# Kernel tuning notes

Hardware: AMD Instinct MI355X
Metric: run time of the kernel (lower is better)

## Reference

```python
import jax, jax.numpy as jnp
import numpy as np


def setup_inputs() -> dict:
    key = jax.random.key(0)
    k1, k2, k3 = jax.random.split(key, 3)
    B, T, D, Uh = 64, 256, 1024, 1024
    x = jax.random.normal(k1, (B, T, D), dtype=jnp.float32)
    W = jax.random.normal(k2, (D, 4 * Uh), dtype=jnp.float32) * 0.02
    U = jax.random.normal(k3, (Uh, 4 * Uh), dtype=jnp.float32) * 0.02
    b = jnp.zeros((4 * Uh,), dtype=jnp.float32)
    return {"x": x, "W": W, "U": U, "b": b}


def _lstm(x, W, U, b):
    # Keras LSTM, inference mode (dropout inactive). Gate order: i, f, c, o.
    B = x.shape[0]
    units = U.shape[0]
    # Precompute input projection for all timesteps: [B,T,4U] -> scan over T.
    xz = jnp.einsum('btd,dg->btg', x, W) + b
    xz = jnp.swapaxes(xz, 0, 1)  # [T,B,4U]

    def step(carry, xz_t):
        h, c = carry
        z = xz_t + h @ U  # [B,4U]
        zi, zf, zg, zo = jnp.split(z, 4, axis=-1)
        i = jax.nn.sigmoid(zi)
        f = jax.nn.sigmoid(zf)
        g = jnp.tanh(zg)
        o = jax.nn.sigmoid(zo)
        c_new = f * c + i * g
        h_new = o * jnp.tanh(c_new)
        return (h_new, c_new), h_new

    h0 = jnp.zeros((B, units), dtype=x.dtype)
    c0 = jnp.zeros((B, units), dtype=x.dtype)
    _, hs = jax.lax.scan(step, (h0, c0), xz)  # hs: [T,B,U]
    return jnp.swapaxes(hs, 0, 1)  # [B,T,U] (return_sequences=True)


def reference(x, W, U, b):
    return _lstm(x, W, U, b)
```

## Files before the change

kernel.cpp:

```cpp
#include <hip/hip_runtime.h>
#include <cstdint>
#include <cstddef>

typedef __attribute__((ext_vector_type(8))) short short8;
typedef __attribute__((ext_vector_type(4))) short short4v;
typedef __attribute__((ext_vector_type(4))) float f32x4;
typedef __attribute__((ext_vector_type(4))) int int4v;

static constexpr int B_ = 64, T_ = 256, D_ = 1024, NH = 1024, NG = 4096;
static constexpr int NBLK = 64;
static constexpr int NWRK = 192;
static constexpr int LDS_BYTES = 131072 + 64 * 68 * 4;
static constexpr uint64_t DLY_TICKS = 50;

__device__ __forceinline__ short f2bs(float f) {
  union { float f; uint32_t u; } cv; cv.f = f;
  uint32_t u = cv.u;
  uint32_t r = (u + 0x7fffu + ((u >> 16) & 1u)) >> 16;
  return (short)(uint16_t)r;
}
__device__ __forceinline__ float bs2f(short s) {
  union { uint32_t u; float f; } cv; cv.u = ((uint32_t)(uint16_t)s) << 16; return cv.f;
}
__device__ __forceinline__ float fsigm(float x) {
  return __builtin_amdgcn_rcpf(1.f + __expf(-x));
}
__device__ __forceinline__ float ftanh(float x) {
  return 1.f - 2.f * __builtin_amdgcn_rcpf(__expf(2.f * x) + 1.f);
}
__device__ __forceinline__ uint64_t rtclock() {
  uint64_t v;
  asm volatile("s_memrealtime %0\n\ts_waitcnt lgkmcnt(0)" : "=s"(v));
  return v;
}

#define WAITV(N) do { asm volatile("s_waitcnt vmcnt(" #N ")" ::: "memory"); \
                      __builtin_amdgcn_sched_barrier(0); } while (0)

#define HL2(B0, B1, VO) \
  asm volatile("global_load_dwordx4 %0, %2, %3 sc0 sc1\n\t" \
               "global_load_dwordx4 %1, %2, %3 offset:16 sc0 sc1" \
               : "=&v"(B0), "=&v"(B1) : "v"(VO), "s"(hpv) : "memory")

#define ISSUE_A { _Pragma("unroll") \
  for (int K = 0; K < 8; ++K) HL2(bufA[2*K], bufA[2*K+1], voff0 + K * 8192); }
#define ISSUE_B { _Pragma("unroll") \
  for (int K = 0; K < 8; ++K) HL2(bufB[2*K], bufB[2*K+1], voff0 + 65536 + K * 8192); }

#define CHECKBUF(BUF) { _Pragma("unroll") \
  for (int i = 0; i < 16; ++i) { \
    bad |= ((uint32_t)BUF[i][0] ^ tgw); bad |= ((uint32_t)BUF[i][1] ^ tgw); \
    bad |= ((uint32_t)BUF[i][2] ^ tgw); bad |= ((uint32_t)BUF[i][3] ^ tgw); \
  } bad &= 0xFFFF0000u; }

#define MFMA_SUB(BUF, KB) { _Pragma("unroll") \
  for (int K = 0; K < 8; ++K) { \
    int4v pk; \
    pk[0] = (BUF[2*K][0]   & 0xFFFF) | (BUF[2*K][1]   << 16); \
    pk[1] = (BUF[2*K][2]   & 0xFFFF) | (BUF[2*K][3]   << 16); \
    pk[2] = (BUF[2*K+1][0] & 0xFFFF) | (BUF[2*K+1][1] << 16); \
    pk[3] = (BUF[2*K+1][2] & 0xFFFF) | (BUF[2*K+1][3] << 16); \
    const short8 fa = __builtin_bit_cast(short8, pk); \
    const int ksAbs = kh * 16 + (KB) + K; \
    _Pragma("unroll") \
    for (int nt = 0; nt < 4; ++nt) { \
      const short8 fb = *reinterpret_cast<const short8*>(&Us[((ksAbs*4 + kg)*64 + nt*16 + fr)*8]); \
      acc[nt] = __builtin_amdgcn_mfma_f32_16x16x32_bf16(fa, fb, acc[nt], 0, 0, 0); \
    } \
  } }

__global__ __launch_bounds__(512, 1) void lstm_fused(
    const float* __restrict__ x, const float* __restrict__ W,
    const float* __restrict__ bias, const float* __restrict__ U,
    short* __restrict__ xzT, uint32_t* __restrict__ h0buf,
    uint32_t* __restrict__ h1buf, int* __restrict__ ready,
    float* __restrict__ out)
{
  extern __shared__ char smem[];
  const int tid  = threadIdx.x;
  const int lane = tid & 63, wave = tid >> 6;
  const int bid  = blockIdx.x;
  const int fr = lane & 15, kg = lane >> 4;

  if (bid >= NBLK) {
    short* As = (short*)smem;
    short* Bs = (short*)(smem + 16384);
    short* Cs = (short*)smem;
    const int wm = (wave >> 2) * 128, wn = (wave & 3) * 64;
    const int fq = lane >> 4;
    const int wid = bid - NBLK;

    for (int tile = wid; tile < 1024; tile += NWRK) {
      const int tt = tile >> 4;
      const int bn = (tile & 15) * 256;
      f32x4 acc[8][4] = {};

      for (int k0 = 0; k0 < D_; k0 += 32) {
        {
          const int r0 = tid >> 3, kq = (tid & 7) * 4;
          #pragma unroll
          for (int it = 0; it < 4; ++it) {
            const int r = r0 + it * 64;
            const int m = tt * 256 + r;
            const int xr = (m & 63) * 256 + (m >> 6);
            const float4 v = *reinterpret_cast<const float4*>(&x[(size_t)xr * D_ + k0 + kq]);
            short4v s; s.x = f2bs(v.x); s.y = f2bs(v.y); s.z = f2bs(v.z); s.w = f2bs(v.w);
            *reinterpret_cast<short4v*>(&As[r * 32 + kq]) = s;
          }
        }
        {
          const int kr0 = tid >> 6, nq = (tid & 63) * 4;
          #pragma unroll
          for (int it = 0; it < 4; ++it) {
            const int krow = kr0 + it * 8;
            const float4 v = *reinterpret_cast<const float4*>(&W[(size_t)(k0 + krow) * NG + bn + nq]);
            short4v s; s.x = f2bs(v.x); s.y = f2bs(v.y); s.z = f2bs(v.z); s.w = f2bs(v.w);
            *reinterpret_cast<short4v*>(&Bs[krow * 256 + nq]) = s;
          }
        }
        __syncthreads();

        short8 af[8];
        #pragma unroll
        for (int mi = 0; mi < 8; ++mi)
          af[mi] = *reinterpret_cast<const short8*>(&As[(wm + mi * 16 + fr) * 32 + kg * 8]);
        #pragma unroll
        for (int ni = 0; ni < 4; ++ni) {
          short8 bf;
          #pragma unroll
          for (int j = 0; j < 8; ++j) bf[j] = Bs[(kg * 8 + j) * 256 + wn + ni * 16 + fr];
          #pragma unroll
          for (int mi = 0; mi < 8; ++mi)
            acc[mi][ni] = __builtin_amdgcn_mfma_f32_16x16x32_bf16(af[mi], bf, acc[mi][ni], 0, 0, 0);
        }
        __syncthreads();
      }

      const int g = bn >> 10, rb0 = (bn & 1023) >> 4;
      #pragma unroll
      for (int hp = 0; hp < 2; ++hp) {
        __syncthreads();
        if ((wave >> 2) == hp) {
          #pragma unroll
          for (int ni = 0; ni < 4; ++ni) {
            const int col = wn + ni * 16 + fr;
            const float bv = bias[bn + col];
            #pragma unroll
            for (int mi = 0; mi < 8; ++mi) {
              const int rowl = mi * 16 + fq * 4;
              #pragma unroll
              for (int r = 0; r < 4; ++r)
                Cs[(rowl + r) * 264 + col] = f2bs(acc[mi][ni][r] + bv);
            }
          }
        }
        __syncthreads();
        #pragma unroll
        for (int it = 0; it < 4; ++it) {
          const int cid = it * 512 + tid;
          const int tl = cid >> 4, rbi = cid & 15;
          const int r = hp * 128 + tl;
          const int t = tt * 4 + (r >> 6);
          const int b = r & 63;
          short* dst = xzT + ((size_t)((rb0 + rbi) * 256 + t) * 64 + b) * 64 + g * 16;
          const int4v v0 = *reinterpret_cast<const int4v*>(&Cs[tl * 264 + rbi * 16]);
          const int4v v1 = *reinterpret_cast<const int4v*>(&Cs[tl * 264 + rbi * 16 + 8]);
          asm volatile("global_store_dwordx4 %0, %1, off sc0 sc1\n\t"
                       "global_store_dwordx4 %0, %2, off offset:16 sc0 sc1"
                       :: "v"(dst), "v"(v0), "v"(v1) : "memory");
        }
      }
      asm volatile("s_waitcnt vmcnt(0)" ::: "memory");
      __syncthreads();
      if (tid == 0)
        __hip_atomic_fetch_add(&ready[tt], 1, __ATOMIC_RELAXED, __HIP_MEMORY_SCOPE_AGENT);
    }
    return;
  }

  short* Us  = (short*)smem;
  float* zsm = (float*)(smem + 131072);

  const int u0 = bid * 16;
  const int mt = wave & 3;
  const int kh = wave >> 2;
  const int gb = tid >> 3, gup = tid & 7;

  for (int idx = tid; idx < 1024 * 64; idx += 512) {
    const int k = idx >> 6, c = idx & 63;
    Us[((k >> 3) * 64 + c) * 8 + (k & 7)] =
        f2bs(U[(size_t)k * NG + (c >> 4) * NH + u0 + (c & 15)]);
  }
  float creg0 = 0.f, creg1 = 0.f;
  const int voff0 = kh * 131072 + kg * 2048 + mt * 512 + fr * 32;
  const int pks = bid >> 1;
  const int pkg = ((bid & 1) << 1) + (gup >> 2);
  const int pj  = (2 * gup) & 7;
  const int pidx = ((pks * 4 + pkg) * 64 + gb) * 8 + pj;
  __syncthreads();
  uint64_t rt0 = rtclock();
  int grpOK = -1;

  for (int t = 0; t < T_; ++t) {
    const uint32_t* __restrict__ hpv = (t & 1) ? h0buf : h1buf;
    uint32_t* __restrict__ hnx       = (t & 1) ? h1buf : h0buf;

    const int grp = t >> 4;
    if (grp > grpOK) {
      if (lane == 0) {
        int spun = 0;
        for (;;) {
          int4v rv;
          asm volatile("global_load_dwordx4 %0, %1, off sc0 sc1\n\t"
                       "s_waitcnt vmcnt(0)"
                       : "=&v"(rv) : "v"(ready + grp * 4) : "memory");
          if (rv[0] == 16 && rv[1] == 16 && rv[2] == 16 && rv[3] == 16) break;
          spun = 1;
          __builtin_amdgcn_s_sleep(16);
        }
        if (spun) {
          #pragma unroll
          for (int s = 0; s < 4; ++s) __builtin_amdgcn_s_sleep(127);
        }
      }
      grpOK = grp;
    }

    int xzw[4];
    {
      const short* xb = xzT + ((((size_t)bid * 256 + t) * 64 + gb) * 64 + 2 * gup);
      asm volatile("global_load_dword %0, %4, off sc0 sc1\n\t"
                   "global_load_dword %1, %4, off offset:32 sc0 sc1\n\t"
                   "global_load_dword %2, %4, off offset:64 sc0 sc1\n\t"
                   "global_load_dword %3, %4, off offset:96 sc0 sc1"
                   : "=&v"(xzw[0]), "=&v"(xzw[1]), "=&v"(xzw[2]), "=&v"(xzw[3])
                   : "v"(xb) : "memory");
    }

    f32x4 acc[4] = {};
    if (t > 0) {
      const uint32_t tgw = (uint32_t)t << 16;
      int4v bufA[16], bufB[16];
      while ((uint64_t)(rtclock() - rt0) < DLY_TICKS)
        __builtin_amdgcn_s_sleep(1);
      ISSUE_A; ISSUE_B;
      WAITV(16);
      for (;;) {
        uint32_t bad = 0; CHECKBUF(bufA);
        if (__all(bad == 0)) break;
        __builtin_amdgcn_s_sleep(4);
        ISSUE_A; WAITV(0);
      }
      MFMA_SUB(bufA, 0);
      WAITV(0);
      for (;;) {
        uint32_t bad = 0; CHECKBUF(bufB);
        if (__all(bad == 0)) break;
        __builtin_amdgcn_s_sleep(4);
        ISSUE_B; WAITV(0);
      }
      MFMA_SUB(bufB, 8);

      if (kh == 1) {
        #pragma unroll
        for (int nt = 0; nt < 4; ++nt)
          #pragma unroll
          for (int r = 0; r < 4; ++r)
            zsm[(mt * 16 + kg * 4 + r) * 68 + nt * 16 + fr] = acc[nt][r];
      }
      __syncthreads();
      if (kh == 0) {
        #pragma unroll
        for (int nt = 0; nt < 4; ++nt)
          #pragma unroll
          for (int r = 0; r < 4; ++r)
            zsm[(mt * 16 + kg * 4 + r) * 68 + nt * 16 + fr] += acc[nt][r];
      }
      __syncthreads();
    } else {
      asm volatile("s_waitcnt vmcnt(0)" ::: "memory");
    }

    {
      float z[4][2];
      #pragma unroll
      for (int g = 0; g < 4; ++g) {
        z[g][0] = bs2f((short)(xzw[g] & 0xFFFF));
        z[g][1] = bs2f((short)(((uint32_t)xzw[g]) >> 16));
        if (t > 0) {
          const float2 zz = *reinterpret_cast<const float2*>(&zsm[gb * 68 + g * 16 + 2 * gup]);
          z[g][0] += zz.x; z[g][1] += zz.y;
        }
      }
      float hh0, hh1;
      {
        const float ig = fsigm(z[0][0]), fg = fsigm(z[1][0]);
        const float gg = ftanh(z[2][0]), og = fsigm(z[3][0]);
        creg0 = fg * creg0 + ig * gg;  hh0 = og * ftanh(creg0);
      }
      {
        const float ig = fsigm(z[0][1]), fg = fsigm(z[1][1]);
        const float gg = ftanh(z[2][1]), og = fsigm(z[3][1]);
        creg1 = fg * creg1 + ig * gg;  hh1 = og * ftanh(creg1);
      }
      if (t < T_ - 1) {
        const uint32_t tgp = (uint32_t)(t + 1) << 16;
        const uint64_t hw64 =
            (uint64_t)(tgp | (uint32_t)(uint16_t)f2bs(hh0)) |
            ((uint64_t)(tgp | (uint32_t)(uint16_t)f2bs(hh1)) << 32);
        (void)__hip_atomic_exchange((uint64_t*)(hnx + pidx), hw64,
                                    __ATOMIC_RELAXED, __HIP_MEMORY_SCOPE_AGENT);
      }
      rt0 = rtclock();
      float2 o; o.x = hh0; o.y = hh1;
      *reinterpret_cast<float2*>(&out[((size_t)gb * T_ + t) * NH + u0 + 2 * gup]) = o;
    }
    __builtin_amdgcn_s_barrier();
  }
}

extern "C" void kernel_launch(void* const* d_in, const int* in_sizes, int n_in,
                              void* d_out, int out_size, void* d_ws, size_t ws_size,
                              hipStream_t stream) {
  const float* x    = (const float*)d_in[0];
  const float* W    = (const float*)d_in[1];
  const float* U    = (const float*)d_in[2];
  const float* bias = (const float*)d_in[3];
  float* out = (float*)d_out;
  char* ws = (char*)d_ws;

  short*    xzT   = (short*)ws;
  uint32_t* hA    = (uint32_t*)(ws + 134217728);
  uint32_t* hB    = (uint32_t*)(ws + 134217728 + 262144);
  int*      ready = (int*)(ws + 134217728 + 524288);

  hipMemsetAsync(ws + 134217728, 0, 524288 + 4096, stream);

  hipFuncSetAttribute((const void*)lstm_fused,
                      hipFuncAttributeMaxDynamicSharedMemorySize, LDS_BYTES);
  lstm_fused<<<dim3(NBLK + NWRK), dim3(512), LDS_BYTES, stream>>>(
      x, W, bias, U, xzT, hA, hB, ready, out);
}
```

Baseline: 1.918 ms.

## Quantize recurrent matmul to int8 and pin recurrent blocks to one XCD

The recurrent weights U and hidden state h move from bf16 to int8, using per-column scales for U and a fixed 127 scale for h, and the step matmul now uses i8 MFMA. This halves the h exchange payload and the LDS footprint. Recurrent roles are claimed dynamically only by blocks running on XCC 0, so all 64 recurrent blocks share one L2 and h reads use non-sc1 loads. The projection GEMM tiles shrink to 128 rows across more worker blocks that later become recurrent roles, and the launch allows 4 blocks per CU. The int8 quantization lowers accuracy, and the role-claim scheme relies on enough blocks landing on XCD 0.

```diff
diff --git a/kernel.cpp b/kernel.cpp
--- a/kernel.cpp
+++ b/kernel.cpp
@@ -6,12 +6,13 @@
 typedef __attribute__((ext_vector_type(4))) short short4v;
 typedef __attribute__((ext_vector_type(4))) float f32x4;
 typedef __attribute__((ext_vector_type(4))) int int4v;
+typedef __attribute__((ext_vector_type(2))) int int2v;
 
 static constexpr int B_ = 64, T_ = 256, D_ = 1024, NH = 1024, NG = 4096;
-static constexpr int NBLK = 64;
-static constexpr int NWRK = 192;
-static constexpr int LDS_BYTES = 131072 + 64 * 68 * 4;
-static constexpr uint64_t DLY_TICKS = 50;
+static constexpr int NROLE = 64;
+static constexpr int NWRK  = 448;
+static constexpr int LDS_BYTES = 65536 + 16384;
+static constexpr uint64_t DLY_TICKS = 25;
 
 __device__ __forceinline__ short f2bs(float f) {
   union { float f; uint32_t u; } cv; cv.f = f;
@@ -37,71 +38,90 @@
 #define WAITV(N) do { asm volatile("s_waitcnt vmcnt(" #N ")" ::: "memory"); \
                       __builtin_amdgcn_sched_barrier(0); } while (0)
 
-#define HL2(B0, B1, VO) \
-  asm volatile("global_load_dwordx4 %0, %2, %3 sc0 sc1\n\t" \
-               "global_load_dwordx4 %1, %2, %3 offset:16 sc0 sc1" \
-               : "=&v"(B0), "=&v"(B1) : "v"(VO), "s"(hpv) : "memory")
-
-#define ISSUE_A { _Pragma("unroll") \
-  for (int K = 0; K < 8; ++K) HL2(bufA[2*K], bufA[2*K+1], voff0 + K * 8192); }
-#define ISSUE_B { _Pragma("unroll") \
-  for (int K = 0; K < 8; ++K) HL2(bufB[2*K], bufB[2*K+1], voff0 + 65536 + K * 8192); }
+#define HLF(B0, VO) \
+  asm volatile("global_load_dwordx4 %0, %1, %2 sc0" \
+               : "=&v"(B0) : "v"(VO), "s"(hpv) : "memory")
+#define HLS(B0, VO) \
+  asm volatile("global_load_dwordx4 %0, %1, %2 sc0 sc1" \
+               : "=&v"(B0) : "v"(VO), "s"(hpv) : "memory")
+
+#define ISSUE_F(BUF, BASE) { _Pragma("unroll") \
+  for (int K = 0; K < 8; ++K) HLF(BUF[K], voff0 + (BASE) + K * 4096); }
+#define ISSUE_S(BUF, BASE) { _Pragma("unroll") \
+  for (int K = 0; K < 8; ++K) HLS(BUF[K], voff0 + (BASE) + K * 4096); }
 
 #define CHECKBUF(BUF) { _Pragma("unroll") \
-  for (int i = 0; i < 16; ++i) { \
+  for (int i = 0; i < 8; ++i) { \
     bad |= ((uint32_t)BUF[i][0] ^ tgw); bad |= ((uint32_t)BUF[i][1] ^ tgw); \
     bad |= ((uint32_t)BUF[i][2] ^ tgw); bad |= ((uint32_t)BUF[i][3] ^ tgw); \
   } bad &= 0xFFFF0000u; }
 
 #define MFMA_SUB(BUF, KB) { _Pragma("unroll") \
   for (int K = 0; K < 8; ++K) { \
-    int4v pk; \
-    pk[0] = (BUF[2*K][0]   & 0xFFFF) | (BUF[2*K][1]   << 16); \
-    pk[1] = (BUF[2*K][2]   & 0xFFFF) | (BUF[2*K][3]   << 16); \
-    pk[2] = (BUF[2*K+1][0] & 0xFFFF) | (BUF[2*K+1][1] << 16); \
-    pk[3] = (BUF[2*K+1][2] & 0xFFFF) | (BUF[2*K+1][3] << 16); \
-    const short8 fa = __builtin_bit_cast(short8, pk); \
+    int2v ad; \
+    ad[0] = (BUF[K][0] & 0xFFFF) | ((BUF[K][1] & 0xFFFF) << 16); \
+    ad[1] = (BUF[K][2] & 0xFFFF) | ((BUF[K][3] & 0xFFFF) << 16); \
+    const long long a64 = __builtin_bit_cast(long long, ad); \
     const int ksAbs = kh * 16 + (KB) + K; \
     _Pragma("unroll") \
     for (int nt = 0; nt < 4; ++nt) { \
-      const short8 fb = *reinterpret_cast<const short8*>(&Us[((ksAbs*4 + kg)*64 + nt*16 + fr)*8]); \
-      acc[nt] = __builtin_amdgcn_mfma_f32_16x16x32_bf16(fa, fb, acc[nt], 0, 0, 0); \
+      const int boff = ((ksAbs * 4 + kg) * 64 + nt * 16 + fr) * 8; \
+      const long long b64 = *reinterpret_cast<const long long*>(Us + boff); \
+      acc[nt] = __builtin_amdgcn_mfma_i32_16x16x32_i8(a64, b64, acc[nt], 0, 0, 0); \
     } \
   } }
 
-__global__ __launch_bounds__(512, 1) void lstm_fused(
+__global__ __launch_bounds__(512, 4) void lstm_mega(
     const float* __restrict__ x, const float* __restrict__ W,
     const float* __restrict__ bias, const float* __restrict__ U,
     short* __restrict__ xzT, uint32_t* __restrict__ h0buf,
     uint32_t* __restrict__ h1buf, int* __restrict__ ready,
-    float* __restrict__ out)
+    int* __restrict__ claim, float* __restrict__ out)
 {
   extern __shared__ char smem[];
   const int tid  = threadIdx.x;
   const int lane = tid & 63, wave = tid >> 6;
-  const int bid  = blockIdx.x;
   const int fr = lane & 15, kg = lane >> 4;
 
-  if (bid >= NBLK) {
+  int* role_sh = (int*)smem;
+  if (tid == 0) {
+    int xcd = 0;
+    asm volatile("s_getreg_b32 %0, hwreg(HW_REG_XCC_ID)" : "=s"(xcd));
+    int r = -1;
+    if ((xcd & 7) == 0)
+      r = __hip_atomic_fetch_add(claim, 1, __ATOMIC_RELAXED, __HIP_MEMORY_SCOPE_AGENT);
+    role_sh[0] = r;
+  }
+  __syncthreads();
+  int role = role_sh[0];
+  __syncthreads();
+
+  if (role < 0 || role >= NROLE) {
     short* As = (short*)smem;
-    short* Bs = (short*)(smem + 16384);
+    short* Bs = (short*)(smem + 8192);
     short* Cs = (short*)smem;
-    const int wm = (wave >> 2) * 128, wn = (wave & 3) * 64;
+    const int wm = (wave >> 2) * 64, wn = (wave & 3) * 64;
     const int fq = lane >> 4;
-    const int wid = bid - NBLK;
-
-    for (int tile = wid; tile < 1024; tile += NWRK) {
-      const int tt = tile >> 4;
+    int wid;
+    if (tid == 0)
+      role_sh[1] = __hip_atomic_fetch_add(claim + 4, 1, __ATOMIC_RELAXED,
+                                          __HIP_MEMORY_SCOPE_AGENT);
+    __syncthreads();
+    wid = role_sh[1];
+    __syncthreads();
+
+    for (int tile = wid; tile < 2048; tile += NWRK) {
+      const int mtile = tile >> 4;
       const int bn = (tile & 15) * 256;
-      f32x4 acc[8][4] = {};
+      f32x4 acc[4][4] = {};
 
       for (int k0 = 0; k0 < D_; k0 += 32) {
         {
           const int r0 = tid >> 3, kq = (tid & 7) * 4;
           #pragma unroll
-          for (int it = 0; it < 4; ++it) {
+          for (int it = 0; it < 2; ++it) {
             const int r = r0 + it * 64;
-            const int m = tt * 256 + r;
+            const int m = mtile * 128 + r;
             const int xr = (m & 63) * 256 + (m >> 6);
             const float4 v = *reinterpret_cast<const float4*>(&x[(size_t)xr * D_ + k0 + kq]);
             short4v s; s.x = f2bs(v.x); s.y = f2bs(v.y); s.z = f2bs(v.z); s.w = f2bs(v.w);
@@ -120,9 +140,9 @@
         }
         __syncthreads();
 
-        short8 af[8];
-        #pragma unroll
-        for (int mi = 0; mi < 8; ++mi)
+        short8 af[4];
+        #pragma unroll
+        for (int mi = 0; mi < 4; ++mi)
           af[mi] = *reinterpret_cast<const short8*>(&As[(wm + mi * 16 + fr) * 32 + kg * 8]);
         #pragma unroll
         for (int ni = 0; ni < 4; ++ni) {
@@ -130,74 +150,88 @@
           #pragma unroll
           for (int j = 0; j < 8; ++j) bf[j] = Bs[(kg * 8 + j) * 256 + wn + ni * 16 + fr];
           #pragma unroll
-          for (int mi = 0; mi < 8; ++mi)
+          for (int mi = 0; mi < 4; ++mi)
             acc[mi][ni] = __builtin_amdgcn_mfma_f32_16x16x32_bf16(af[mi], bf, acc[mi][ni], 0, 0, 0);
         }
         __syncthreads();
       }
 
       const int g = bn >> 10, rb0 = (bn & 1023) >> 4;
+      __syncthreads();
       #pragma unroll
-      for (int hp = 0; hp < 2; ++hp) {
-        __syncthreads();
-        if ((wave >> 2) == hp) {
-          #pragma unroll
-          for (int ni = 0; ni < 4; ++ni) {
-            const int col = wn + ni * 16 + fr;
-            const float bv = bias[bn + col];
-            #pragma unroll
-            for (int mi = 0; mi < 8; ++mi) {
-              const int rowl = mi * 16 + fq * 4;
-              #pragma unroll
-              for (int r = 0; r < 4; ++r)
-                Cs[(rowl + r) * 264 + col] = f2bs(acc[mi][ni][r] + bv);
-            }
-          }
-        }
-        __syncthreads();
-        #pragma unroll
-        for (int it = 0; it < 4; ++it) {
-          const int cid = it * 512 + tid;
-          const int tl = cid >> 4, rbi = cid & 15;
-          const int r = hp * 128 + tl;
-          const int t = tt * 4 + (r >> 6);
-          const int b = r & 63;
-          short* dst = xzT + ((size_t)((rb0 + rbi) * 256 + t) * 64 + b) * 64 + g * 16;
-          const int4v v0 = *reinterpret_cast<const int4v*>(&Cs[tl * 264 + rbi * 16]);
-          const int4v v1 = *reinterpret_cast<const int4v*>(&Cs[tl * 264 + rbi * 16 + 8]);
-          asm volatile("global_store_dwordx4 %0, %1, off sc0 sc1\n\t"
-                       "global_store_dwordx4 %0, %2, off offset:16 sc0 sc1"
-                       :: "v"(dst), "v"(v0), "v"(v1) : "memory");
-        }
+      for (int ni = 0; ni < 4; ++ni) {
+        const int col = wn + ni * 16 + fr;
+        const float bv = bias[bn + col];
+        #pragma unroll
+        for (int mi = 0; mi < 4; ++mi) {
+          const int rowl = wm + mi * 16 + (lane >> 4) * 4;
+          #pragma unroll
+          for (int r = 0; r < 4; ++r)
+            Cs[(rowl + r) * 264 + col] = f2bs(acc[mi][ni][r] + bv);
+        }
+      }
+      __syncthreads();
+      #pragma unroll
+      for (int it = 0; it < 4; ++it) {
+        const int cid = it * 512 + tid;
+        const int rl = cid >> 4, rbi = cid & 15;
+        const int t = mtile * 2 + (rl >> 6);
+        const int b = rl & 63;
+        short* dst = xzT + ((size_t)((rb0 + rbi) * 256 + t) * 64 + b) * 64 + g * 16;
+        const int4v v0 = *reinterpret_cast<const int4v*>(&Cs[rl * 264 + rbi * 16]);
+        const int4v v1 = *reinterpret_cast<const int4v*>(&Cs[rl * 264 + rbi * 16 + 8]);
+        asm volatile("global_store_dwordx4 %0, %1, off sc0 sc1\n\t"
+                     "global_store_dwordx4 %0, %2, off offset:16 sc0 sc1"
+                     :: "v"(dst), "v"(v0), "v"(v1) : "memory");
       }
       asm volatile("s_waitcnt vmcnt(0)" ::: "memory");
       __syncthreads();
       if (tid == 0)
-        __hip_atomic_fetch_add(&ready[tt], 1, __ATOMIC_RELAXED, __HIP_MEMORY_SCOPE_AGENT);
-    }
-    return;
-  }
-
-  short* Us  = (short*)smem;
-  float* zsm = (float*)(smem + 131072);
-
-  const int u0 = bid * 16;
+        __hip_atomic_fetch_add(&ready[mtile >> 1], 1, __ATOMIC_RELAXED,
+                               __HIP_MEMORY_SCOPE_AGENT);
+      __syncthreads();
+    }
+
+    if (tid == 0)
+      role_sh[0] = __hip_atomic_fetch_add(claim, 1, __ATOMIC_RELAXED,
+                                          __HIP_MEMORY_SCOPE_AGENT);
+    __syncthreads();
+    role = role_sh[0];
+    __syncthreads();
+    if (role < 0 || role >= NROLE) return;
+  }
+
+  char*  Us  = smem;
+  float* zsm = (float*)(smem + 65536);
+
+  const int u0 = role * 16;
   const int mt = wave & 3;
   const int kh = wave >> 2;
   const int gb = tid >> 3, gup = tid & 7;
 
+  if (tid < 64) {
+    float m = 1e-30f;
+    for (int k = 0; k < 1024; ++k)
+      m = fmaxf(m, fabsf(U[(size_t)k * NG + (tid >> 4) * NH + u0 + (tid & 15)]));
+    zsm[tid] = m;
+    zsm[64 + tid] = 127.f / m;
+  }
+  __syncthreads();
   for (int idx = tid; idx < 1024 * 64; idx += 512) {
     const int k = idx >> 6, c = idx & 63;
-    Us[((k >> 3) * 64 + c) * 8 + (k & 7)] =
-        f2bs(U[(size_t)k * NG + (c >> 4) * NH + u0 + (c & 15)]);
-  }
+    const float v = U[(size_t)k * NG + (c >> 4) * NH + u0 + (c & 15)];
+    const int q = (int)rintf(v * zsm[64 + c]);
+    Us[(((k >> 5) * 4 + ((k >> 3) & 3)) * 64 + c) * 8 + (k & 7)] = (char)q;
+  }
+  float sdiv[4];
+  #pragma unroll
+  for (int nt = 0; nt < 4; ++nt) sdiv[nt] = zsm[nt * 16 + fr] * (1.f / 16129.f);
+  __syncthreads();
+
   float creg0 = 0.f, creg1 = 0.f;
-  const int voff0 = kh * 131072 + kg * 2048 + mt * 512 + fr * 32;
-  const int pks = bid >> 1;
-  const int pkg = ((bid & 1) << 1) + (gup >> 2);
-  const int pj  = (2 * gup) & 7;
-  const int pidx = ((pks * 4 + pkg) * 64 + gb) * 8 + pj;
-  __syncthreads();
+  const int voff0 = kh * 65536 + kg * 1024 + (mt * 16 + fr) * 16;
+  const int uu = u0 + 2 * gup;
+  const int pidx = (((uu >> 5) * 4 + ((uu >> 3) & 3)) * 64 + gb) * 4 + ((uu >> 1) & 3);
   uint64_t rt0 = rtclock();
   int grpOK = -1;
 
@@ -214,7 +248,7 @@
           asm volatile("global_load_dwordx4 %0, %1, off sc0 sc1\n\t"
                        "s_waitcnt vmcnt(0)"
                        : "=&v"(rv) : "v"(ready + grp * 4) : "memory");
-          if (rv[0] == 16 && rv[1] == 16 && rv[2] == 16 && rv[3] == 16) break;
+          if (rv[0] >= 32 && rv[1] >= 32 && rv[2] >= 32 && rv[3] >= 32) break;
           spun = 1;
           __builtin_amdgcn_s_sleep(16);
         }
@@ -228,7 +262,7 @@
 
     int xzw[4];
     {
-      const short* xb = xzT + ((((size_t)bid * 256 + t) * 64 + gb) * 64 + 2 * gup);
+      const short* xb = xzT + ((((size_t)role * 256 + t) * 64 + gb) * 64 + 2 * gup);
       asm volatile("global_load_dword %0, %4, off sc0 sc1\n\t"
                    "global_load_dword %1, %4, off offset:32 sc0 sc1\n\t"
                    "global_load_dword %2, %4, off offset:64 sc0 sc1\n\t"
@@ -237,27 +271,35 @@
                    : "v"(xb) : "memory");
     }
 
-    f32x4 acc[4] = {};
+    int4v acc[4] = {};
     if (t > 0) {
       const uint32_t tgw = (uint32_t)t << 16;
-      int4v bufA[16], bufB[16];
+      int4v bufA[8], bufB[8];
       while ((uint64_t)(rtclock() - rt0) < DLY_TICKS)
         __builtin_amdgcn_s_sleep(1);
-      ISSUE_A; ISSUE_B;
-      WAITV(16);
-      for (;;) {
-        uint32_t bad = 0; CHECKBUF(bufA);
-        if (__all(bad == 0)) break;
-        __builtin_amdgcn_s_sleep(4);
-        ISSUE_A; WAITV(0);
+      ISSUE_F(bufA, 0); ISSUE_F(bufB, 32768);
+      WAITV(8);
+      {
+        int tries = 0;
+        for (;;) {
+          uint32_t bad = 0; CHECKBUF(bufA);
+          if (__all(bad == 0)) break;
+          __builtin_amdgcn_s_sleep(2);
+          if (++tries < 6) { ISSUE_F(bufA, 0); } else { ISSUE_S(bufA, 0); }
+          WAITV(0);
+        }
       }
       MFMA_SUB(bufA, 0);
       WAITV(0);
-      for (;;) {
-        uint32_t bad = 0; CHECKBUF(bufB);
-        if (__all(bad == 0)) break;
-        __builtin_amdgcn_s_sleep(4);
-        ISSUE_B; WAITV(0);
+      {
+        int tries = 0;
+        for (;;) {
+          uint32_t bad = 0; CHECKBUF(bufB);
+          if (__all(bad == 0)) break;
+          __builtin_amdgcn_s_sleep(2);
+          if (++tries < 6) { ISSUE_F(bufB, 32768); } else { ISSUE_S(bufB, 32768); }
+          WAITV(0);
+        }
       }
       MFMA_SUB(bufB, 8);
 
@@ -266,7 +308,7 @@
         for (int nt = 0; nt < 4; ++nt)
           #pragma unroll
           for (int r = 0; r < 4; ++r)
-            zsm[(mt * 16 + kg * 4 + r) * 68 + nt * 16 + fr] = acc[nt][r];
+            zsm[(mt * 16 + kg * 4 + r) * 64 + nt * 16 + fr] = (float)acc[nt][r] * sdiv[nt];
       }
       __syncthreads();
       if (kh == 0) {
@@ -274,7 +316,7 @@
         for (int nt = 0; nt < 4; ++nt)
           #pragma unroll
           for (int r = 0; r < 4; ++r)
-            zsm[(mt * 16 + kg * 4 + r) * 68 + nt * 16 + fr] += acc[nt][r];
+            zsm[(mt * 16 + kg * 4 + r) * 64 + nt * 16 + fr] += (float)acc[nt][r] * sdiv[nt];
       }
       __syncthreads();
     } else {
@@ -288,7 +330,7 @@
         z[g][0] = bs2f((short)(xzw[g] & 0xFFFF));
         z[g][1] = bs2f((short)(((uint32_t)xzw[g]) >> 16));
         if (t > 0) {
-          const float2 zz = *reinterpret_cast<const float2*>(&zsm[gb * 68 + g * 16 + 2 * gup]);
+          const float2 zz = *reinterpret_cast<const float2*>(&zsm[gb * 64 + g * 16 + 2 * gup]);
           z[g][0] += zz.x; z[g][1] += zz.y;
         }
       }
@@ -304,12 +346,14 @@
         creg1 = fg * creg1 + ig * gg;  hh1 = og * ftanh(creg1);
       }
       if (t < T_ - 1) {
-        const uint32_t tgp = (uint32_t)(t + 1) << 16;
-        const uint64_t hw64 =
-            (uint64_t)(tgp | (uint32_t)(uint16_t)f2bs(hh0)) |
-            ((uint64_t)(tgp | (uint32_t)(uint16_t)f2bs(hh1)) << 32);
-        (void)__hip_atomic_exchange((uint64_t*)(hnx + pidx), hw64,
-                                    __ATOMIC_RELAXED, __HIP_MEMORY_SCOPE_AGENT);
+        const int q0 = (int)rintf(hh0 * 127.f);
+        const int q1 = (int)rintf(hh1 * 127.f);
+        const uint32_t word = ((uint32_t)(t + 1) << 16) |
+                              (((uint32_t)q1 & 0xFF) << 8) | ((uint32_t)q0 & 0xFF);
+        uint32_t* hp32 = hnx + pidx;
+        asm volatile("global_store_dword %0, %1, off sc0\n\t"
+                     "global_store_dword %0, %1, off sc0 sc1"
+                     :: "v"(hp32), "v"(word) : "memory");
       }
       rt0 = rtclock();
       float2 o; o.x = hh0; o.y = hh1;
@@ -331,13 +375,14 @@
 
   short*    xzT   = (short*)ws;
   uint32_t* hA    = (uint32_t*)(ws + 134217728);
-  uint32_t* hB    = (uint32_t*)(ws + 134217728 + 262144);
-  int*      ready = (int*)(ws + 134217728 + 524288);
-
-  hipMemsetAsync(ws + 134217728, 0, 524288 + 4096, stream);
-
-  hipFuncSetAttribute((const void*)lstm_fused,
+  uint32_t* hB    = (uint32_t*)(ws + 134217728 + 131072);
+  int*      ready = (int*)(ws + 134217728 + 262144);
+  int*      claim = (int*)(ws + 134217728 + 262144 + 4096);
+
+  hipMemsetAsync(ws + 134217728, 0, 262144 + 4096 + 64, stream);
+
+  hipFuncSetAttribute((const void*)lstm_mega,
                       hipFuncAttributeMaxDynamicSharedMemorySize, LDS_BYTES);
-  lstm_fused<<<dim3(NBLK + NWRK), dim3(512), LDS_BYTES, stream>>>(
-      x, W, bias, U, xzT, hA, hB, ready, out);
-}
+  lstm_mega<<<dim3(512), dim3(512), LDS_BYTES, stream>>>(
+      x, W, bias, U, xzT, hA, hB, ready, claim, out);
+}
```

Measured after the change: 6.306 ms. 229% more time.
